# Optimization experiments

Measured on AMD Instinct MI355X. Metric: run time of the kernel, lower is better.

## Reference

```python
import jax, jax.numpy as jnp
from jax import lax
import numpy as np

B, N, C, NPOINT, K = 8, 4096, 64, 1024, 32
EPS = 1e-5
SLOPE = 0.1  # leakyrelu negative_slope


def setup_inputs() -> dict:
    key = jax.random.key(0)
    ks = jax.random.split(key, 8)
    d = {
        "xyz": jax.random.normal(ks[0], (B, N, 3), jnp.float32),
        "features": jax.random.normal(ks[1], (B, N, C), jnp.float32),
    }
    for i, n in enumerate(["w_t", "w1_0", "w2_0", "w1_1", "w2_1"]):
        d[n] = jax.random.normal(ks[2 + i], (C, C), jnp.float32) * 0.05
    for n in ["b_t", "b1_0", "b2_0", "b1_1", "b2_1"]:
        d[n] = jnp.zeros((C,), jnp.float32)
    for n in ["g_t", "g1_0", "g2_0", "g1_1", "g2_1"]:
        d[n] = jnp.ones((C,), jnp.float32)
    for n in ["beta_t", "beta1_0", "beta2_0", "beta1_1", "beta2_1"]:
        d[n] = jnp.zeros((C,), jnp.float32)
    return d


def leaky(x):
    return jnp.where(x >= 0, x, SLOPE * x)


def conv1(x, w, b):  # x: [M, Cin, K], w: [Cout, Cin] (1x1 conv)
    return jnp.einsum('mck,oc->mok', x, w) + b[None, :, None]


def bn(x, g, be):  # training-mode BatchNorm1d over (batch, spatial)
    mean = x.mean(axis=(0, 2), keepdims=True)
    var = x.var(axis=(0, 2), keepdims=True)
    return g[None, :, None] * (x - mean) / jnp.sqrt(var + EPS) + be[None, :, None]


def fps(xyz, npoint):
    """Farthest point sampling, deterministic start at index 0. -> [B, npoint] int32"""
    b, n, _ = xyz.shape
    def step(carry, _):
        dist, far = carry
        centroid = jnp.take_along_axis(xyz, far[:, None, None], axis=1)  # [B,1,3]
        d = jnp.sum((xyz - centroid) ** 2, -1)  # [B,N]
        dist = jnp.minimum(dist, d)
        return (dist, jnp.argmax(dist, -1)), far
    init = (jnp.full((b, n), 1e10, xyz.dtype), jnp.zeros((b,), jnp.int32))
    _, idxs = lax.scan(step, init, None, length=npoint)  # [npoint, B]
    return idxs.T


def sqdist(src, dst):  # [B,S,3],[B,N,3] -> [B,S,N]
    d = -2.0 * jnp.einsum('bsc,bnc->bsn', src, dst)
    d += jnp.sum(src ** 2, -1)[:, :, None]
    d += jnp.sum(dst ** 2, -1)[:, None, :]
    return d


def resblock(x, w1, b1, g1, be1, w2, b2, g2, be2):
    h = leaky(bn(conv1(x, w1, b1), g1, be1))
    h = bn(conv1(h, w2, b2), g2, be2)
    return leaky(h + x)


def reference(xyz, features, w_t, b_t, g_t, beta_t,
              w1_0, b1_0, g1_0, beta1_0, w2_0, b2_0, g2_0, beta2_0,
              w1_1, b1_1, g1_1, beta1_1, w2_1, b2_1, g2_1, beta2_1):
    fps_idx = fps(xyz, NPOINT)                                   # [B,S]
    new_xyz = jnp.take_along_axis(xyz, fps_idx[:, :, None], axis=1)  # [B,S,3]
    d = sqdist(new_xyz, xyz)                                     # [B,S,N]
    _, idx = lax.top_k(-d, K)                                    # k smallest -> [B,S,K]
    grouped = jax.vmap(lambda f, i: f[i])(features, idx)         # [B,S,K,C]
    x = grouped.transpose(0, 1, 3, 2).reshape(B * NPOINT, C, K)  # [B*S, C, K]
    x = leaky(bn(conv1(x, w_t, b_t), g_t, beta_t))
    x = resblock(x, w1_0, b1_0, g1_0, beta1_0, w2_0, b2_0, g2_0, beta2_0)
    x = resblock(x, w1_1, b1_1, g1_1, beta1_1, w2_1, b2_1, g2_1, beta2_1)
    nf = x.reshape(B, NPOINT, C, K).transpose(0, 2, 1, 3)        # [B,C,S,K]
    sub_features = nf.max(axis=-1)                               # [B,C,S]
    return (new_xyz.transpose(0, 2, 1), sub_features)
```

## Files before the change

kernel.cpp:

```cpp
#include <hip/hip_runtime.h>
#include <stdint.h>

#define NB 8
#define NN 4096
#define NC 64
#define NS 1024
#define NK 32
#define NQ (NB*NS)
#define NP (NQ*NK)
#define EPSBN 1e-5f

typedef unsigned long long u64;
typedef unsigned short u16;
typedef float v2f __attribute__((ext_vector_type(2)));
typedef short bf8_t __attribute__((ext_vector_type(8)));
typedef float f4_t __attribute__((ext_vector_type(4)));

__device__ __forceinline__ float lrelu(float x){ return x >= 0.0f ? x : 0.1f*x; }

__device__ __forceinline__ unsigned int fkey(float d){
    unsigned int fb = __float_as_uint(d);
    return (fb & 0x80000000u) ? ~fb : (fb | 0x80000000u);
}
__device__ __forceinline__ unsigned f2bf(float f){
    unsigned u = __float_as_uint(f);
    return (u + 0x7fffu + ((u >> 16) & 1u)) >> 16;
}
__device__ __forceinline__ float bflo(unsigned u){ return __uint_as_float(u << 16); }
__device__ __forceinline__ float bfhi(unsigned u){ return __uint_as_float(u & 0xffff0000u); }

__device__ __forceinline__ int wave_incl_add(int x){
    int v = x;
    {int o=__builtin_amdgcn_update_dpp(0,v,0x111,0xf,0xf,true); v+=o;}
    {int o=__builtin_amdgcn_update_dpp(0,v,0x112,0xf,0xf,true); v+=o;}
    {int o=__builtin_amdgcn_update_dpp(0,v,0x114,0xf,0xf,true); v+=o;}
    {int o=__builtin_amdgcn_update_dpp(0,v,0x118,0xf,0xf,true); v+=o;}
    {int o=__builtin_amdgcn_update_dpp(0,v,0x142,0xa,0xf,true); v+=o;}
    {int o=__builtin_amdgcn_update_dpp(0,v,0x143,0xc,0xf,true); v+=o;}
    return v;
}
__device__ __forceinline__ float row_sum16(float x){
    int v = __float_as_int(x);
    {int o=__builtin_amdgcn_update_dpp(0,v,0x111,0xf,0xf,true); v=__float_as_int(__int_as_float(v)+__int_as_float(o));}
    {int o=__builtin_amdgcn_update_dpp(0,v,0x112,0xf,0xf,true); v=__float_as_int(__int_as_float(v)+__int_as_float(o));}
    {int o=__builtin_amdgcn_update_dpp(0,v,0x114,0xf,0xf,true); v=__float_as_int(__int_as_float(v)+__int_as_float(o));}
    {int o=__builtin_amdgcn_update_dpp(0,v,0x118,0xf,0xf,true); v=__float_as_int(__int_as_float(v)+__int_as_float(o));}
    return __int_as_float(v);
}
__device__ __forceinline__ double wave_max_d(double x){
    int lo = __double2loint(x), hi = __double2hiint(x);
    #define FPS_STG(ctl) { \
        int nl=__builtin_amdgcn_update_dpp(lo,lo,ctl,0xf,0xf,false); \
        int nh=__builtin_amdgcn_update_dpp(hi,hi,ctl,0xf,0xf,false); \
        double mx=fmax(__hiloint2double(hi,lo), __hiloint2double(nh,nl)); \
        lo=__double2loint(mx); hi=__double2hiint(mx); }
    FPS_STG(0x111) FPS_STG(0x112) FPS_STG(0x114) FPS_STG(0x118) FPS_STG(0x142) FPS_STG(0x143)
    #undef FPS_STG
    int flo = __builtin_amdgcn_readlane(lo, 63);
    int fhi = __builtin_amdgcn_readlane(hi, 63);
    return __hiloint2double(fhi, flo);
}

__global__ __launch_bounds__(256,1) void fps_kernel(const float* __restrict__ xyz,
                                                    float* __restrict__ out0,
                                                    float* __restrict__ nxyz)
{
    __shared__ float sX[NN], sY[NN], sZ[NN];
    __shared__ double slots[2][4];
    __shared__ int sFar[NS];
    const int b = blockIdx.x, t = threadIdx.x;
    const int lane = t & 63, wv = t >> 6;
    const float* base = xyz + (size_t)b*NN*3;
    for (int i = t; i < NN; i += 256){
        const float* pp = base + 3*i;
        sX[i] = pp[0]; sY[i] = pp[1]; sZ[i] = pp[2];
    }
    __syncthreads();
    v2f PX[8], PY[8], PZ[8], D[8];
    int LO[16];
    const int pb = t*16;
    #pragma unroll
    for (int j = 0; j < 8; ++j){
        PX[j] = (v2f){ sX[pb+2*j], sX[pb+2*j+1] };
        PY[j] = (v2f){ sY[pb+2*j], sY[pb+2*j+1] };
        PZ[j] = (v2f){ sZ[pb+2*j], sZ[pb+2*j+1] };
        D[j]  = (v2f){ 1e10f, 1e10f };
    }
    #pragma unroll
    for (int j = 0; j < 16; ++j) LO[j] = (int)(~(unsigned)(pb + j));
    int far = 0;
    float cx = sX[0], cy = sY[0], cz = sZ[0];
    for (int s = 0; s < NS; ++s){
        if (t == 255) sFar[s] = far;
        double best;
        {
            #pragma clang fp contract(off)
            v2f cx2 = (v2f){cx, cx}, cy2 = (v2f){cy, cy}, cz2 = (v2f){cz, cz};
            best = -1.0;
            #pragma unroll
            for (int j = 0; j < 8; ++j){
                v2f dx = PX[j] - cx2;
                v2f dy = PY[j] - cy2;
                v2f dz = PZ[j] - cz2;
                v2f dd = (dx*dx + dy*dy) + dz*dz;
                v2f nd = __builtin_elementwise_min(D[j], dd);
                D[j] = nd;
                best = fmax(best, __hiloint2double(__float_as_int(nd.x), LO[2*j]));
                best = fmax(best, __hiloint2double(__float_as_int(nd.y), LO[2*j+1]));
            }
        }
        double wb = wave_max_d(best);
        const int par = s & 1;
        if (lane == 0) slots[par][wv] = wb;
        __syncthreads();
        double s0 = slots[par][0], s1 = slots[par][1];
        double s2 = slots[par][2], s3 = slots[par][3];
        double mm = fmax(fmax(s0, s1), fmax(s2, s3));
        far = (int)(~(unsigned)__double2loint(mm));
        cx = sX[far]; cy = sY[far]; cz = sZ[far];
    }
    __syncthreads();
    for (int s = t; s < NS; s += 256){
        const int f = sFar[s];
        const float x = sX[f], y = sY[f], z = sZ[f];
        float* npq = nxyz + ((size_t)b*NS + s)*3;
        npq[0]=x; npq[1]=y; npq[2]=z;
        out0[(b*3+0)*NS+s]=x; out0[(b*3+1)*NS+s]=y; out0[(b*3+2)*NS+s]=z;
    }
}

__global__ __launch_bounds__(256,2) void knn_kernel(const float* __restrict__ xyz,
                                                    const float* __restrict__ nxyz,
                                                    int* __restrict__ kidx)
{
    const int t = threadIdx.x, lane = t & 63, w = t >> 6;
    const int q = blockIdx.x*4 + w;
    const int b = q >> 10;
    const float* base = xyz + (size_t)b*NN*3;
    const float* qp = nxyz + (size_t)q*3;
    const float qx = qp[0], qy = qp[1], qz = qp[2];
    const float qsq = __fadd_rn(__fadd_rn(__fmul_rn(qx,qx),__fmul_rn(qy,qy)),__fmul_rn(qz,qz));

    unsigned int key[64];
    #pragma unroll
    for (int i = 0; i < 64; ++i){
        const int idx = (i<<6) + lane;
        const float* pp = base + 3*idx;
        float x = pp[0], y = pp[1], z = pp[2];
        float dot = __fadd_rn(__fadd_rn(__fmul_rn(qx,x),__fmul_rn(qy,y)),__fmul_rn(qz,z));
        float psq = __fadd_rn(__fadd_rn(__fmul_rn(x,x),__fmul_rn(y,y)),__fmul_rn(z,z));
        float d = __fadd_rn(__fadd_rn(__fmul_rn(-2.0f,dot),qsq),psq);
        key[i] = fkey(d);
    }
    unsigned int pref = 0; int need = 32;
    for (int bit = 31; bit >= 0; --bit){
        const unsigned int bound = 1u << bit;
        int c = 0;
        #pragma unroll
        for (int i = 0; i < 64; ++i) c += ((key[i] ^ pref) < bound) ? 1 : 0;
        int tot = __builtin_amdgcn_readlane(wave_incl_add(c), 63);
        if (tot < need){ need -= tot; pref |= bound; }
    }
    const unsigned int T = pref;
    int cl = 0;
    #pragma unroll
    for (int i = 0; i < 64; ++i) cl += (key[i] < T) ? 1 : 0;
    int incl_cl = wave_incl_add(cl);
    int clx = incl_cl - cl;
    int tiebase = __builtin_amdgcn_readlane(incl_cl, 63);
    int* oq = kidx + (size_t)q*NK;
    int pos = clx;
    #pragma unroll
    for (int i = 0; i < 64; ++i){
        if (key[i] < T){ oq[pos] = (i<<6) + lane; ++pos; }
    }
    int tcount = 0;
    for (int i = 0; i < 64 && tcount < need; ++i){
        u64 m = __ballot(key[i] == T);
        int myrank = (int)__popcll(m & ((1ull << lane) - 1ull));
        if ((key[i] == T) && (tcount + myrank < need))
            oq[tiebase + tcount + myrank] = (i<<6) + lane;
        tcount += (int)__popcll(m);
    }
}

__global__ __launch_bounds__(256) void wtrans_kernel(const float* __restrict__ w0,
    const float* __restrict__ w1, const float* __restrict__ w2,
    const float* __restrict__ w3, const float* __restrict__ w4,
    u16* __restrict__ dst)
{
    const float* s;
    switch (blockIdx.x){
        case 0: s = w0; break; case 1: s = w1; break; case 2: s = w2; break;
        case 3: s = w3; break; default: s = w4; break;
    }
    u16* d = dst + (size_t)blockIdx.x*4096;
    for (int i = threadIdx.x; i < 4096; i += 256){
        const int f = i >> 9, lane = (i >> 3) & 63, j = i & 7;
        const int mt = f >> 1, h = f & 1;
        const int o = mt*16 + (lane & 15);
        const int c = h*32 + (lane >> 4)*8 + j;
        d[i] = (u16)f2bf(s[o*64 + c]);
    }
}

template<int ACT>
__global__ __launch_bounds__(256,3) void conv_mfma_kernel(const u16* __restrict__ in,
    u16* __restrict__ out, const u16* __restrict__ wfrag, const float* __restrict__ bias,
    const float* __restrict__ pin, const float* __restrict__ g,
    const float* __restrict__ beta, float* __restrict__ affout,
    float* __restrict__ pout)
{
    __shared__ float sPS[128];
    __shared__ float sAff[128];
    __shared__ float sStat[4*128];
    const int t = threadIdx.x, lane = t & 63, wv = t >> 6;
    const int n = lane & 15, q = lane >> 4;
    const int bb = blockIdx.x;

    if (ACT){
        if (t < 128){
            float S = 0.0f;
            #pragma unroll 8
            for (int r = 0; r < 512; ++r) S += pin[r*128 + t];
            sPS[t] = S;
        }
        __syncthreads();
        if (t < 64){
            float mean = sPS[t] * (1.0f/(float)NP);
            float var  = fmaxf(sPS[64+t] * (1.0f/(float)NP) - mean*mean, 0.0f);
            float sc = g[t] * rsqrtf(var + EPSBN);
            sAff[t]    = sc;
            sAff[64+t] = beta[t] - mean*sc;
            if (affout){ affout[t] = sc; affout[64+t] = sAff[64+t]; }
        }
        __syncthreads();
    }
    float scr[16], shr[16];
    if (ACT){
        #pragma unroll
        for (int h = 0; h < 2; ++h)
            #pragma unroll
            for (int j = 0; j < 8; ++j){
                const int k = h*32 + q*8 + j;
                scr[h*8+j] = sAff[k]; shr[h*8+j] = sAff[64+k];
            }
    }
    bf8_t wf[8];
    #pragma unroll
    for (int f = 0; f < 8; ++f)
        wf[f] = *(const bf8_t*)(wfrag + (f*64 + lane)*8);
    f4_t bv[4];
    #pragma unroll
    for (int mt = 0; mt < 4; ++mt)
        bv[mt] = *(const f4_t*)(bias + mt*16 + q*4);

    float st1[16], st2[16];
    #pragma unroll
    for (int e = 0; e < 16; ++e){ st1[e] = 0.0f; st2[e] = 0.0f; }

    for (int i = 0; i < 8; ++i){
        const int p0 = bb*512 + wv*128 + i*16;
        const u16* row = in + (size_t)(p0 + n)*64;
        bf8_t bf0, bf1;
        if (ACT){
            union { unsigned u[4]; bf8_t v; } B0, B1;
            uint4 r0 = *(const uint4*)(row + q*8);
            uint4 r1 = *(const uint4*)(row + 32 + q*8);
            const unsigned ra[4] = {r0.x, r0.y, r0.z, r0.w};
            const unsigned rb[4] = {r1.x, r1.y, r1.z, r1.w};
            #pragma unroll
            for (int d = 0; d < 4; ++d){
                float x0 = bflo(ra[d]), x1 = bfhi(ra[d]);
                float y0 = fmaf(scr[2*d],   x0, shr[2*d]);   y0 = lrelu(y0);
                float y1 = fmaf(scr[2*d+1], x1, shr[2*d+1]); y1 = lrelu(y1);
                B0.u[d] = f2bf(y0) | (f2bf(y1) << 16);
                float z0 = bflo(rb[d]), z1 = bfhi(rb[d]);
                float w0 = fmaf(scr[8+2*d],   z0, shr[8+2*d]);   w0 = lrelu(w0);
                float w1 = fmaf(scr[8+2*d+1], z1, shr[8+2*d+1]); w1 = lrelu(w1);
                B1.u[d] = f2bf(w0) | (f2bf(w1) << 16);
            }
            bf0 = B0.v; bf1 = B1.v;
        } else {
            bf0 = *(const bf8_t*)(row + q*8);
            bf1 = *(const bf8_t*)(row + 32 + q*8);
        }
        f4_t acc[4];
        #pragma unroll
        for (int mt = 0; mt < 4; ++mt){
            acc[mt] = (f4_t){0.f,0.f,0.f,0.f};
            acc[mt] = __builtin_amdgcn_mfma_f32_16x16x32_bf16(wf[mt*2+0], bf0, acc[mt], 0,0,0);
            acc[mt] = __builtin_amdgcn_mfma_f32_16x16x32_bf16(wf[mt*2+1], bf1, acc[mt], 0,0,0);
        }
        u16* orow = out + (size_t)(p0 + n)*64;
        #pragma unroll
        for (int mt = 0; mt < 4; ++mt){
            float v0 = acc[mt].x + bv[mt].x;
            float v1 = acc[mt].y + bv[mt].y;
            float v2 = acc[mt].z + bv[mt].z;
            float v3 = acc[mt].w + bv[mt].w;
            st1[mt*4+0] += v0; st2[mt*4+0] += v0*v0;
            st1[mt*4+1] += v1; st2[mt*4+1] += v1*v1;
            st1[mt*4+2] += v2; st2[mt*4+2] += v2*v2;
            st1[mt*4+3] += v3; st2[mt*4+3] += v3*v3;
            uint2 pk;
            pk.x = f2bf(v0) | (f2bf(v1) << 16);
            pk.y = f2bf(v2) | (f2bf(v3) << 16);
            *(uint2*)(orow + mt*16 + q*4) = pk;
        }
    }
    #pragma unroll
    for (int e = 0; e < 16; ++e){
        float r1 = row_sum16(st1[e]);
        float r2 = row_sum16(st2[e]);
        if (n == 15){
            const int ch = (e >> 2)*16 + q*4 + (e & 3);
            sStat[wv*128 + ch]      = r1;
            sStat[wv*128 + 64 + ch] = r2;
        }
    }
    __syncthreads();
    if (t < 128){
        float s = sStat[t] + sStat[128+t] + sStat[256+t] + sStat[384+t];
        pout[(size_t)bb*128 + t] = s;
    }
}

__global__ __launch_bounds__(256,3) void gconv_mfma_kernel(const float* __restrict__ features,
    const int* __restrict__ kidx, u16* __restrict__ out,
    const u16* __restrict__ wfrag, const float* __restrict__ bias,
    float* __restrict__ pout)
{
    __shared__ float sStat[4*128];
    const int t = threadIdx.x, lane = t & 63, wv = t >> 6;
    const int n = lane & 15, q = lane >> 4;
    const int bb = blockIdx.x;

    bf8_t wf[8];
    #pragma unroll
    for (int f = 0; f < 8; ++f)
        wf[f] = *(const bf8_t*)(wfrag + (f*64 + lane)*8);
    f4_t bv[4];
    #pragma unroll
    for (int mt = 0; mt < 4; ++mt)
        bv[mt] = *(const f4_t*)(bias + mt*16 + q*4);

    float st1[16], st2[16];
    #pragma unroll
    for (int e = 0; e < 16; ++e){ st1[e] = 0.0f; st2[e] = 0.0f; }

    for (int i = 0; i < 8; ++i){
        const int p0 = bb*512 + wv*128 + i*16;
        const int p = p0 + n;
        const int b = p >> 15;
        const int idx = kidx[p];
        const float* frow = features + ((size_t)b*NN + idx)*NC;
        union { unsigned u[4]; bf8_t v; } B0, B1;
        {
            float4 a0 = *(const float4*)(frow + q*8);
            float4 a1 = *(const float4*)(frow + q*8 + 4);
            B0.u[0] = f2bf(a0.x) | (f2bf(a0.y) << 16);
            B0.u[1] = f2bf(a0.z) | (f2bf(a0.w) << 16);
            B0.u[2] = f2bf(a1.x) | (f2bf(a1.y) << 16);
            B0.u[3] = f2bf(a1.z) | (f2bf(a1.w) << 16);
            float4 c0 = *(const float4*)(frow + 32 + q*8);
            float4 c1 = *(const float4*)(frow + 32 + q*8 + 4);
            B1.u[0] = f2bf(c0.x) | (f2bf(c0.y) << 16);
            B1.u[1] = f2bf(c0.z) | (f2bf(c0.w) << 16);
            B1.u[2] = f2bf(c1.x) | (f2bf(c1.y) << 16);
            B1.u[3] = f2bf(c1.z) | (f2bf(c1.w) << 16);
        }
        f4_t acc[4];
        #pragma unroll
        for (int mt = 0; mt < 4; ++mt){
            acc[mt] = (f4_t){0.f,0.f,0.f,0.f};
            acc[mt] = __builtin_amdgcn_mfma_f32_16x16x32_bf16(wf[mt*2+0], B0.v, acc[mt], 0,0,0);
            acc[mt] = __builtin_amdgcn_mfma_f32_16x16x32_bf16(wf[mt*2+1], B1.v, acc[mt], 0,0,0);
        }
        u16* orow = out + (size_t)p*64;
        #pragma unroll
        for (int mt = 0; mt < 4; ++mt){
            float v0 = acc[mt].x + bv[mt].x;
            float v1 = acc[mt].y + bv[mt].y;
            float v2 = acc[mt].z + bv[mt].z;
            float v3 = acc[mt].w + bv[mt].w;
            st1[mt*4+0] += v0; st2[mt*4+0] += v0*v0;
            st1[mt*4+1] += v1; st2[mt*4+1] += v1*v1;
            st1[mt*4+2] += v2; st2[mt*4+2] += v2*v2;
            st1[mt*4+3] += v3; st2[mt*4+3] += v3*v3;
            uint2 pk;
            pk.x = f2bf(v0) | (f2bf(v1) << 16);
            pk.y = f2bf(v2) | (f2bf(v3) << 16);
            *(uint2*)(orow + mt*16 + q*4) = pk;
        }
    }
    #pragma unroll
    for (int e = 0; e < 16; ++e){
        float r1 = row_sum16(st1[e]);
        float r2 = row_sum16(st2[e]);
        if (n == 15){
            const int ch = (e >> 2)*16 + q*4 + (e & 3);
            sStat[wv*128 + ch]      = r1;
            sStat[wv*128 + 64 + ch] = r2;
        }
    }
    __syncthreads();
    if (t < 128){
        float s = sStat[t] + sStat[128+t] + sStat[256+t] + sStat[384+t];
        pout[(size_t)bb*128 + t] = s;
    }
}

__global__ __launch_bounds__(128) void finalize_kernel(const float* __restrict__ pin,
    const float* __restrict__ g, const float* __restrict__ beta, float* __restrict__ aff)
{
    __shared__ float sPS[128];
    const int t = threadIdx.x;
    float S = 0.0f;
    #pragma unroll 8
    for (int r = 0; r < 512; ++r) S += pin[r*128 + t];
    sPS[t] = S;
    __syncthreads();
    if (t < 64){
        float mean = sPS[t] * (1.0f/(float)NP);
        float var  = fmaxf(sPS[64+t] * (1.0f/(float)NP) - mean*mean, 0.0f);
        float sc = g[t] * rsqrtf(var + EPSBN);
        aff[t]    = sc;
        aff[64+t] = beta[t] - mean*sc;
    }
}

__global__ __launch_bounds__(256,2) void resid_kernel(const u16* __restrict__ v,
    const u16* __restrict__ yt, u16* __restrict__ x2,
    const float* __restrict__ affV, const float* __restrict__ affY)
{
    const int t = threadIdx.x;
    const int dc = t & 31, rg = t >> 5;
    const int c0 = dc*2, c1 = c0 + 1;
    const float va0 = affV[c0], vb0 = affV[64+c0];
    const float va1 = affV[c1], vb1 = affV[64+c1];
    const float ya0 = affY[c0], yb0 = affY[64+c0];
    const float ya1 = affY[c1], yb1 = affY[64+c1];
    const unsigned* vp = (const unsigned*)v;
    const unsigned* yp = (const unsigned*)yt;
    unsigned* xp = (unsigned*)x2;
    const size_t base = (size_t)blockIdx.x*512;
    #pragma unroll 4
    for (int r = rg; r < 512; r += 8){
        const size_t e = (base + r)*32 + dc;
        unsigned uv = vp[e], uy = yp[e];
        float r0 = lrelu(fmaf(va0, bflo(uv), vb0) + lrelu(fmaf(ya0, bflo(uy), yb0)));
        float r1 = lrelu(fmaf(va1, bfhi(uv), vb1) + lrelu(fmaf(ya1, bfhi(uy), yb1)));
        xp[e] = f2bf(r0) | (f2bf(r1) << 16);
    }
}

__global__ __launch_bounds__(256,2) void final_kernel(const u16* __restrict__ v2,
    const u16* __restrict__ x2, const float* __restrict__ aff,
    float* __restrict__ out1)
{
    const int t = threadIdx.x;
    const int dc = t & 31, sg = t >> 5;
    const int c0 = dc*2, c1 = c0 + 1;
    const float a0 = aff[c0], s0 = aff[64+c0];
    const float a1 = aff[c1], s1 = aff[64+c1];
    const int s = blockIdx.x*8 + sg;
    const unsigned* vp = (const unsigned*)v2;
    const unsigned* xp = (const unsigned*)x2;
    float m0 = -3.0e38f, m1 = -3.0e38f;
    #pragma unroll 8
    for (int kk = 0; kk < 32; ++kk){
        const size_t e = ((size_t)s*32 + kk)*32 + dc;
        unsigned uv = vp[e], ux = xp[e];
        m0 = fmaxf(m0, lrelu(fmaf(a0, bflo(uv), s0) + bflo(ux)));
        m1 = fmaxf(m1, lrelu(fmaf(a1, bfhi(uv), s1) + bfhi(ux)));
    }
    const int b = s >> 10, sl = s & 1023;
    out1[((size_t)b*NC + c0)*NS + sl] = m0;
    out1[((size_t)b*NC + c1)*NS + sl] = m1;
}

extern "C" void kernel_launch(void* const* d_in, const int* in_sizes, int n_in,
                              void* d_out, int out_size, void* d_ws, size_t ws_size,
                              hipStream_t stream)
{
    const float* xyz      = (const float*)d_in[0];
    const float* features = (const float*)d_in[1];
    const float* w_t    = (const float*)d_in[2];
    const float* w1_0   = (const float*)d_in[3];
    const float* w2_0   = (const float*)d_in[4];
    const float* w1_1   = (const float*)d_in[5];
    const float* w2_1   = (const float*)d_in[6];
    const float* b_t    = (const float*)d_in[7];
    const float* b1_0   = (const float*)d_in[8];
    const float* b2_0   = (const float*)d_in[9];
    const float* b1_1   = (const float*)d_in[10];
    const float* b2_1   = (const float*)d_in[11];
    const float* g_t    = (const float*)d_in[12];
    const float* g1_0   = (const float*)d_in[13];
    const float* g2_0   = (const float*)d_in[14];
    const float* g1_1   = (const float*)d_in[15];
    const float* g2_1   = (const float*)d_in[16];
    const float* beta_t  = (const float*)d_in[17];
    const float* beta1_0 = (const float*)d_in[18];
    const float* beta2_0 = (const float*)d_in[19];
    const float* beta1_1 = (const float*)d_in[20];
    const float* beta2_1 = (const float*)d_in[21];

    float* out = (float*)d_out;

    float* nxyz = (float*)d_ws;
    int*   kidx = (int*)(nxyz + 24576);
    float* pT   = (float*)(kidx + NP);
    float* p10  = pT  + 65536;
    float* p20  = p10 + 65536;
    float* p11  = p20 + 65536;
    float* p21  = p11 + 65536;
    float* affT  = p21 + 65536;
    float* aff20 = affT + 128;
    float* aff21 = aff20 + 128;
    u16*  bwt  = (u16*)(aff21 + 128);
    u16*  buf0 = bwt + 5*4096;
    u16*  buf1 = buf0 + (size_t)NP*NC;
    u16*  buf2 = buf1 + (size_t)NP*NC;

    wtrans_kernel<<<5, 256, 0, stream>>>(w_t, w1_0, w2_0, w1_1, w2_1, bwt);
    fps_kernel<<<NB, 256, 0, stream>>>(xyz, out, nxyz);
    knn_kernel<<<NQ/4, 256, 0, stream>>>(xyz, nxyz, kidx);

    gconv_mfma_kernel<<<512, 256, 0, stream>>>(features, kidx, buf1,
                                               bwt + 0*4096, b_t, pT);
    conv_mfma_kernel<1><<<512, 256, 0, stream>>>(buf1, buf0, bwt + 1*4096, b1_0,
                                                 pT, g_t, beta_t, affT, p10);
    conv_mfma_kernel<1><<<512, 256, 0, stream>>>(buf0, buf2, bwt + 2*4096, b2_0,
                                                 p10, g1_0, beta1_0, nullptr, p20);
    finalize_kernel<<<1, 128, 0, stream>>>(p20, g2_0, beta2_0, aff20);
    resid_kernel<<<512, 256, 0, stream>>>(buf2, buf1, buf0, aff20, affT);
    conv_mfma_kernel<0><<<512, 256, 0, stream>>>(buf0, buf1, bwt + 3*4096, b1_1,
                                                 nullptr, nullptr, nullptr, nullptr, p11);
    conv_mfma_kernel<1><<<512, 256, 0, stream>>>(buf1, buf2, bwt + 4*4096, b2_1,
                                                 p11, g1_1, beta1_1, nullptr, p21);
    finalize_kernel<<<1, 128, 0, stream>>>(p21, g2_1, beta2_1, aff21);
    final_kernel<<<1024, 256, 0, stream>>>(buf2, buf0, aff21,
                                           out + (size_t)NB*3*NS);
}
```

Baseline: 978.0 us.

## Widen FPS to 512 threads and hoist BN stat reduction into parallel finalize

The FPS kernel now uses 512 threads per batch, so each thread owns 8 points instead of 16 and the cross-wave argmax reads 8 slots. This shortens the per-iteration serial work at the cost of more waves joining each barrier. The BN statistics reduction that every conv block used to redo redundantly (512 rows summed per block) moves into a separate 1024-thread finalize kernel that splits the sum across 8 segments. Conv kernels now just load precomputed affine parameters. This adds extra kernel launches between the convs.

```diff
diff --git a/kernel.cpp b/kernel.cpp
--- a/kernel.cpp
+++ b/kernel.cpp
@@ -61,44 +61,44 @@
     return __hiloint2double(fhi, flo);
 }
 
-__global__ __launch_bounds__(256,1) void fps_kernel(const float* __restrict__ xyz,
+__global__ __launch_bounds__(512,1) void fps_kernel(const float* __restrict__ xyz,
                                                     float* __restrict__ out0,
                                                     float* __restrict__ nxyz)
 {
     __shared__ float sX[NN], sY[NN], sZ[NN];
-    __shared__ double slots[2][4];
+    __shared__ double slots[2][8];
     __shared__ int sFar[NS];
     const int b = blockIdx.x, t = threadIdx.x;
     const int lane = t & 63, wv = t >> 6;
     const float* base = xyz + (size_t)b*NN*3;
-    for (int i = t; i < NN; i += 256){
+    for (int i = t; i < NN; i += 512){
         const float* pp = base + 3*i;
         sX[i] = pp[0]; sY[i] = pp[1]; sZ[i] = pp[2];
     }
     __syncthreads();
-    v2f PX[8], PY[8], PZ[8], D[8];
-    int LO[16];
-    const int pb = t*16;
-    #pragma unroll
-    for (int j = 0; j < 8; ++j){
+    v2f PX[4], PY[4], PZ[4], D[4];
+    int LO[8];
+    const int pb = t*8;
+    #pragma unroll
+    for (int j = 0; j < 4; ++j){
         PX[j] = (v2f){ sX[pb+2*j], sX[pb+2*j+1] };
         PY[j] = (v2f){ sY[pb+2*j], sY[pb+2*j+1] };
         PZ[j] = (v2f){ sZ[pb+2*j], sZ[pb+2*j+1] };
         D[j]  = (v2f){ 1e10f, 1e10f };
     }
     #pragma unroll
-    for (int j = 0; j < 16; ++j) LO[j] = (int)(~(unsigned)(pb + j));
+    for (int j = 0; j < 8; ++j) LO[j] = (int)(~(unsigned)(pb + j));
     int far = 0;
     float cx = sX[0], cy = sY[0], cz = sZ[0];
     for (int s = 0; s < NS; ++s){
-        if (t == 255) sFar[s] = far;
+        if (t == 511) sFar[s] = far;
         double best;
         {
             #pragma clang fp contract(off)
             v2f cx2 = (v2f){cx, cx}, cy2 = (v2f){cy, cy}, cz2 = (v2f){cz, cz};
             best = -1.0;
             #pragma unroll
-            for (int j = 0; j < 8; ++j){
+            for (int j = 0; j < 4; ++j){
                 v2f dx = PX[j] - cx2;
                 v2f dy = PY[j] - cy2;
                 v2f dz = PZ[j] - cz2;
@@ -115,12 +115,15 @@
         __syncthreads();
         double s0 = slots[par][0], s1 = slots[par][1];
         double s2 = slots[par][2], s3 = slots[par][3];
-        double mm = fmax(fmax(s0, s1), fmax(s2, s3));
+        double s4 = slots[par][4], s5 = slots[par][5];
+        double s6 = slots[par][6], s7 = slots[par][7];
+        double mm = fmax(fmax(fmax(s0,s1), fmax(s2,s3)),
+                         fmax(fmax(s4,s5), fmax(s6,s7)));
         far = (int)(~(unsigned)__double2loint(mm));
         cx = sX[far]; cy = sY[far]; cz = sZ[far];
     }
     __syncthreads();
-    for (int s = t; s < NS; s += 256){
+    for (int s = t; s < NS; s += 512){
         const int f = sFar[s];
         const float x = sX[f], y = sY[f], z = sZ[f];
         float* npq = nxyz + ((size_t)b*NS + s)*3;
@@ -204,47 +207,55 @@
     }
 }
 
+__global__ __launch_bounds__(1024) void finalize_kernel(const float* __restrict__ pin,
+    const float* __restrict__ g, const float* __restrict__ beta, float* __restrict__ aff)
+{
+    __shared__ float l1[1024];
+    const int t = threadIdx.x;
+    const int stat = t & 127, seg = t >> 7;
+    float S = 0.0f;
+    #pragma unroll 8
+    for (int r = seg*64; r < seg*64 + 64; ++r) S += pin[r*128 + stat];
+    l1[t] = S;
+    __syncthreads();
+    if (t < 128){
+        float s = l1[t] + l1[128+t] + l1[256+t] + l1[384+t]
+                + l1[512+t] + l1[640+t] + l1[768+t] + l1[896+t];
+        l1[t] = s;
+    }
+    __syncthreads();
+    if (t < 64){
+        float mean = l1[t] * (1.0f/(float)NP);
+        float var  = fmaxf(l1[64+t] * (1.0f/(float)NP) - mean*mean, 0.0f);
+        float sc = g[t] * rsqrtf(var + EPSBN);
+        aff[t]    = sc;
+        aff[64+t] = beta[t] - mean*sc;
+    }
+}
+
 template<int ACT>
 __global__ __launch_bounds__(256,3) void conv_mfma_kernel(const u16* __restrict__ in,
     u16* __restrict__ out, const u16* __restrict__ wfrag, const float* __restrict__ bias,
-    const float* __restrict__ pin, const float* __restrict__ g,
-    const float* __restrict__ beta, float* __restrict__ affout,
-    float* __restrict__ pout)
-{
-    __shared__ float sPS[128];
-    __shared__ float sAff[128];
+    const float* __restrict__ aff, float* __restrict__ pout)
+{
     __shared__ float sStat[4*128];
     const int t = threadIdx.x, lane = t & 63, wv = t >> 6;
     const int n = lane & 15, q = lane >> 4;
     const int bb = blockIdx.x;
 
-    if (ACT){
-        if (t < 128){
-            float S = 0.0f;
-            #pragma unroll 8
-            for (int r = 0; r < 512; ++r) S += pin[r*128 + t];
-            sPS[t] = S;
-        }
-        __syncthreads();
-        if (t < 64){
-            float mean = sPS[t] * (1.0f/(float)NP);
-            float var  = fmaxf(sPS[64+t] * (1.0f/(float)NP) - mean*mean, 0.0f);
-            float sc = g[t] * rsqrtf(var + EPSBN);
-            sAff[t]    = sc;
-            sAff[64+t] = beta[t] - mean*sc;
-            if (affout){ affout[t] = sc; affout[64+t] = sAff[64+t]; }
-        }
-        __syncthreads();
-    }
     float scr[16], shr[16];
     if (ACT){
         #pragma unroll
-        for (int h = 0; h < 2; ++h)
-            #pragma unroll
-            for (int j = 0; j < 8; ++j){
-                const int k = h*32 + q*8 + j;
-                scr[h*8+j] = sAff[k]; shr[h*8+j] = sAff[64+k];
-            }
+        for (int h = 0; h < 2; ++h){
+            float4 a0 = *(const float4*)(aff + h*32 + q*8);
+            float4 a1 = *(const float4*)(aff + h*32 + q*8 + 4);
+            float4 b0 = *(const float4*)(aff + 64 + h*32 + q*8);
+            float4 b1 = *(const float4*)(aff + 64 + h*32 + q*8 + 4);
+            scr[h*8+0]=a0.x; scr[h*8+1]=a0.y; scr[h*8+2]=a0.z; scr[h*8+3]=a0.w;
+            scr[h*8+4]=a1.x; scr[h*8+5]=a1.y; scr[h*8+6]=a1.z; scr[h*8+7]=a1.w;
+            shr[h*8+0]=b0.x; shr[h*8+1]=b0.y; shr[h*8+2]=b0.z; shr[h*8+3]=b0.w;
+            shr[h*8+4]=b1.x; shr[h*8+5]=b1.y; shr[h*8+6]=b1.z; shr[h*8+7]=b1.w;
+        }
     }
     bf8_t wf[8];
     #pragma unroll
@@ -411,25 +422,6 @@
     }
 }
 
-__global__ __launch_bounds__(128) void finalize_kernel(const float* __restrict__ pin,
-    const float* __restrict__ g, const float* __restrict__ beta, float* __restrict__ aff)
-{
-    __shared__ float sPS[128];
-    const int t = threadIdx.x;
-    float S = 0.0f;
-    #pragma unroll 8
-    for (int r = 0; r < 512; ++r) S += pin[r*128 + t];
-    sPS[t] = S;
-    __syncthreads();
-    if (t < 64){
-        float mean = sPS[t] * (1.0f/(float)NP);
-        float var  = fmaxf(sPS[64+t] * (1.0f/(float)NP) - mean*mean, 0.0f);
-        float sc = g[t] * rsqrtf(var + EPSBN);
-        aff[t]    = sc;
-        aff[64+t] = beta[t] - mean*sc;
-    }
-}
-
 __global__ __launch_bounds__(256,2) void resid_kernel(const u16* __restrict__ v,
     const u16* __restrict__ yt, u16* __restrict__ x2,
     const float* __restrict__ affV, const float* __restrict__ affY)
@@ -517,30 +509,35 @@
     float* p11  = p20 + 65536;
     float* p21  = p11 + 65536;
     float* affT  = p21 + 65536;
-    float* aff20 = affT + 128;
-    float* aff21 = aff20 + 128;
+    float* aff10 = affT + 128;
+    float* aff20 = aff10 + 128;
+    float* aff11 = aff20 + 128;
+    float* aff21 = aff11 + 128;
     u16*  bwt  = (u16*)(aff21 + 128);
     u16*  buf0 = bwt + 5*4096;
     u16*  buf1 = buf0 + (size_t)NP*NC;
     u16*  buf2 = buf1 + (size_t)NP*NC;
 
     wtrans_kernel<<<5, 256, 0, stream>>>(w_t, w1_0, w2_0, w1_1, w2_1, bwt);
-    fps_kernel<<<NB, 256, 0, stream>>>(xyz, out, nxyz);
+    fps_kernel<<<NB, 512, 0, stream>>>(xyz, out, nxyz);
     knn_kernel<<<NQ/4, 256, 0, stream>>>(xyz, nxyz, kidx);
 
     gconv_mfma_kernel<<<512, 256, 0, stream>>>(features, kidx, buf1,
                                                bwt + 0*4096, b_t, pT);
+    finalize_kernel<<<1, 1024, 0, stream>>>(pT, g_t, beta_t, affT);
     conv_mfma_kernel<1><<<512, 256, 0, stream>>>(buf1, buf0, bwt + 1*4096, b1_0,
-                                                 pT, g_t, beta_t, affT, p10);
+                                                 affT, p10);
+    finalize_kernel<<<1, 1024, 0, stream>>>(p10, g1_0, beta1_0, aff10);
     conv_mfma_kernel<1><<<512, 256, 0, stream>>>(buf0, buf2, bwt + 2*4096, b2_0,
-                                                 p10, g1_0, beta1_0, nullptr, p20);
-    finalize_kernel<<<1, 128, 0, stream>>>(p20, g2_0, beta2_0, aff20);
+                                                 aff10, p20);
+    finalize_kernel<<<1, 1024, 0, stream>>>(p20, g2_0, beta2_0, aff20);
     resid_kernel<<<512, 256, 0, stream>>>(buf2, buf1, buf0, aff20, affT);
     conv_mfma_kernel<0><<<512, 256, 0, stream>>>(buf0, buf1, bwt + 3*4096, b1_1,
-                                                 nullptr, nullptr, nullptr, nullptr, p11);
+                                                 nullptr, p11);
+    finalize_kernel<<<1, 1024, 0, stream>>>(p11, g1_1, beta1_1, aff11);
     conv_mfma_kernel<1><<<512, 256, 0, stream>>>(buf1, buf2, bwt + 4*4096, b2_1,
-                                                 p11, g1_1, beta1_1, nullptr, p21);
-    finalize_kernel<<<1, 128, 0, stream>>>(p21, g2_1, beta2_1, aff21);
+                                                 aff11, p21);
+    finalize_kernel<<<1, 1024, 0, stream>>>(p21, g2_1, beta2_1, aff21);
     final_kernel<<<1024, 256, 0, stream>>>(buf2, buf0, aff21,
                                            out + (size_t)NB*3*NS);
 }
```

New measurement: 967.7 us. Within noise of the previous version (-1.1%).
